# Performance work log

Hardware: AMD Instinct MI355X
Metric: run time of the kernel (lower is better)

The kernel has to match this reference:

```python
import jax, jax.numpy as jnp
import numpy as np

REALSHAPE = (32, 256, 256)   # even dims required
SHAPE = (32, 256, 129)       # rfft half-spectrum shape
MIDS = (16, 128, 128)
KCUT = 4
B, C = 4, 3


def _hs_np(f):
    # numpy mirror of Fourier.hermitian_symmetric (used only to build the constant feed mask)
    m0, m1, m2 = MIDS
    f = f.copy()
    f[m0+1:, 0, 0] = f[1:m0, 0, 0][::-1].conj()
    f[m0+1:, 0, m2] = f[1:m0, 0, m2][::-1].conj()
    f[m0+1:, m1, 0] = f[1:m0, m1, 0][::-1].conj()
    f[m0+1:, m1, m2] = f[1:m0, m1, m2][::-1].conj()
    f[0, m1+1:, 0] = f[0, 1:m1, 0][::-1].conj()
    f[0, m1+1:, m2] = f[0, 1:m1, m2][::-1].conj()
    f[m0, m1+1:, 0] = f[m0, 1:m1, 0][::-1].conj()
    f[m0, m1+1:, m2] = f[m0, 1:m1, m2][::-1].conj()
    f[m0+1:, m1+1:, 0] = f[1:m0, 1:m1, 0][::-1, ::-1].conj()
    f[m0+1:, 1:m1, 0] = f[1:m0, m1+1:, 0][::-1, ::-1].conj()
    f[m0+1:, m1+1:, m2] = f[1:m0, 1:m1, m2][::-1, ::-1].conj()
    f[m0+1:, 1:m1, m2] = f[1:m0, m1+1:, m2][::-1, ::-1].conj()
    return f


def _constants():
    ks = [np.fft.fftfreq(d, 1.0 / d) for d in SHAPE[:-1]] + [np.arange(SHAPE[-1])]
    kgrid = np.array(np.meshgrid(*ks, indexing='ij'))
    ksq = np.sum(kgrid ** 2, axis=0)
    holders = np.stack(np.meshgrid(*[np.arange(d) for d in SHAPE], indexing='ij'))
    same = np.all(np.stack([_hs_np(h) for h in holders]) == holders, axis=0)
    rem = same & (ksq <= KCUT ** 2)
    feed = np.stack([rem, rem.copy()])
    m0, m1, m2 = MIDS
    for idx in [(0, 0, 0), (0, 0, m2), (0, m1, 0), (0, m1, m2),
                (m0, 0, 0), (m0, 0, m2), (m0, m1, 0), (m0, m1, m2)]:
        feed[(1,) + idx] = False  # purely real corner modes
    feed_idx = np.nonzero(feed.reshape(-1))[0].astype(np.int32)
    ks_sel = np.stack([ksq, ksq])[feed]  # dimscale = (1,1,1)
    Pk = (1.0 / (ks_sel + 1.0) * float(np.prod(REALSHAPE))).astype(np.float32)
    grid = np.stack(np.meshgrid(*[np.arange(d) for d in REALSHAPE], indexing='ij')).astype(np.float32)
    return feed_idx, Pk, grid


def setup_inputs() -> dict:
    feed_idx, Pk, grid = _constants()
    key = jax.random.key(0)
    k1, k2 = jax.random.split(key)
    fr = jax.random.normal(k1, (B, C) + REALSHAPE, jnp.float32)
    seeds = jax.random.normal(k2, (1, 3 * feed_idx.size), jnp.float32)
    return {
        'fr': fr,
        'seeds': seeds,
        'Pk': jnp.asarray(Pk),
        'defscale': jnp.ones(3, jnp.float32),  # defscale / dimscale
        'grid': jnp.asarray(grid),
        'feed_idx': jnp.asarray(feed_idx),
    }


def _hs(f):
    # jax hermitian-symmetrize the rfft half-spectrum (writes are non-overlapping with reads)
    m0, m1, m2 = MIDS
    fl = lambda a: jnp.flip(a, 0).conj()
    fl2 = lambda a: jnp.flip(a, (0, 1)).conj()
    f = f.at[m0+1:, 0, 0].set(fl(f[1:m0, 0, 0]))
    f = f.at[m0+1:, 0, m2].set(fl(f[1:m0, 0, m2]))
    f = f.at[m0+1:, m1, 0].set(fl(f[1:m0, m1, 0]))
    f = f.at[m0+1:, m1, m2].set(fl(f[1:m0, m1, m2]))
    f = f.at[0, m1+1:, 0].set(fl(f[0, 1:m1, 0]))
    f = f.at[0, m1+1:, m2].set(fl(f[0, 1:m1, m2]))
    f = f.at[m0, m1+1:, 0].set(fl(f[m0, 1:m1, 0]))
    f = f.at[m0, m1+1:, m2].set(fl(f[m0, 1:m1, m2]))
    f = f.at[m0+1:, m1+1:, 0].set(fl2(f[1:m0, 1:m1, 0]))
    f = f.at[m0+1:, 1:m1, 0].set(fl2(f[1:m0, m1+1:, 0]))
    f = f.at[m0+1:, m1+1:, m2].set(fl2(f[1:m0, 1:m1, m2]))
    f = f.at[m0+1:, 1:m1, m2].set(fl2(f[1:m0, m1+1:, m2]))
    return f


def _forward(fr, seeds, Pk, defscale, grid, feed_idx):
    fdim = feed_idx.shape[0]
    # scale sparse coefficients by the power spectrum
    x = seeds.reshape(3, fdim) * Pk[None, :] * defscale[:, None]
    # scatter into the (2, *SHAPE) re/im spectrum via flat indices
    nfull = 2 * int(np.prod(SHAPE))
    arr = jnp.zeros((3, nfull), jnp.float32).at[:, feed_idx].set(x).reshape(3, 2, *SHAPE)
    comp = (arr[:, 0] + 1j * arr[:, 1]).astype(jnp.complex64)
    comp = jax.vmap(_hs)(comp)
    disp = jnp.fft.irfftn(comp[None], s=REALSHAPE, axes=(2, 3, 4))  # (1,3,D,H,W) float32
    D, H, W = REALSHAPE
    norm = (jnp.asarray(REALSHAPE, jnp.float32) - 1.0)[None, :, None, None, None]
    moved = 2.0 * ((grid[None] - disp) / norm) - 1.0  # normalized coords in [-1,1]
    gz, gy, gx = moved[0, 0], moved[0, 1], moved[0, 2]  # torch grid channel order [2,1,0] -> (x=W, y=H, z=D)
    # grid_sample: bilinear, padding_mode='border' (clamp float coords), align_corners=True
    fz = jnp.clip((gz + 1.0) * 0.5 * (D - 1), 0.0, D - 1)
    fy = jnp.clip((gy + 1.0) * 0.5 * (H - 1), 0.0, H - 1)
    fx = jnp.clip((gx + 1.0) * 0.5 * (W - 1), 0.0, W - 1)
    z0 = jnp.floor(fz); y0 = jnp.floor(fy); x0 = jnp.floor(fx)
    wz = fz - z0; wy = fy - y0; wx = fx - x0  # (D,H,W), broadcast against (B,C,D,H,W)
    z0i = z0.astype(jnp.int32); z1i = jnp.minimum(z0i + 1, D - 1)
    y0i = y0.astype(jnp.int32); y1i = jnp.minimum(y0i + 1, H - 1)
    x0i = x0.astype(jnp.int32); x1i = jnp.minimum(x0i + 1, W - 1)
    g = lambda zi, yi, xi: fr[:, :, zi, yi, xi]  # gather -> (B,C,D,H,W)
    c00 = g(z0i, y0i, x0i) * (1 - wx) + g(z0i, y0i, x1i) * wx
    c01 = g(z0i, y1i, x0i) * (1 - wx) + g(z0i, y1i, x1i) * wx
    c10 = g(z1i, y0i, x0i) * (1 - wx) + g(z1i, y0i, x1i) * wx
    c11 = g(z1i, y1i, x0i) * (1 - wx) + g(z1i, y1i, x1i) * wx
    c0 = c00 * (1 - wy) + c01 * wy
    c1 = c10 * (1 - wy) + c11 * wy
    return c0 * (1 - wz) + c1 * wz


def reference(fr, seeds, Pk, defscale, grid, feed_idx):
    return _forward(fr, seeds, Pk, defscale, grid, feed_idx)
```

## Files before the change

### kernel.cpp

```cpp
#include <hip/hip_runtime.h>
#include <math.h>

#define D0 32
#define D1 256
#define D2 256
#define HS2 129
#define NVOX (D0*D1*D2)
#define KMAX 4
#define NK 9
#define NK2 5
#define NCH 3
#define BATCH 4
#define FCH 3
#define NBC (BATCH*FCH)
#define C_FLOATS (NCH*NK*NK*NK2*2)

__global__ __launch_bounds__(256) void build_S(
    const float* __restrict__ seeds, const float* __restrict__ Pk,
    const float* __restrict__ defscale, const int* __restrict__ feed_idx,
    int fdim, float* __restrict__ S)
{
    __shared__ float C[C_FLOATS];
    __shared__ int fed[NK*NK];
    int t = threadIdx.x;
    for (int i = t; i < C_FLOATS; i += 256) C[i] = 0.0f;
    if (t < NK*NK) fed[t] = 0;
    __syncthreads();
    float ds0 = defscale[0], ds1 = defscale[1], ds2 = defscale[2];
    const int STR_RI = D0 * D1 * HS2;
    const int STR_A  = D1 * HS2;
    for (int j = t; j < fdim; j += 256) {
        int idx = feed_idx[j];
        int ri = idx / STR_RI; int r = idx - ri * STR_RI;
        int a  = r / STR_A;    r -= a * STR_A;
        int b  = r / HS2;      int c = r - b * HS2;
        int k0 = (a < D0/2) ? a : a - D0;
        int k1 = (b < D1/2) ? b : b - D1;
        if (k0 < -KMAX || k0 > KMAX || k1 < -KMAX || k1 > KMAX || c > KMAX) continue;
        int i0 = k0 + KMAX, i1 = k1 + KMAX;
        float pk = Pk[j];
        int base = ((i0*NK + i1)*NK2 + c)*2 + ri;
        C[base]                 = seeds[0*fdim + j] * pk * ds0;
        C[base + 1*NK*NK*NK2*2] = seeds[1*fdim + j] * pk * ds1;
        C[base + 2*NK*NK*NK2*2] = seeds[2*fdim + j] * pk * ds2;
        if (c == 0) fed[i0*NK + i1] = 1;
    }
    __syncthreads();
    if (t < NK*NK && !fed[t]) {
        int i0 = t / NK, i1 = t - i0*NK;
        int m0 = (NK-1) - i0, m1 = (NK-1) - i1;
        for (int ch = 0; ch < NCH; ++ch) {
            int dst = ((ch*NK*NK + i0*NK + i1)*NK2 + 0)*2;
            int src = ((ch*NK*NK + m0*NK + m1)*NK2 + 0)*2;
            C[dst]   = C[src];
            C[dst+1] = -C[src+1];
        }
    }
    __syncthreads();

    int zyl = t >> 3;
    int g   = t & 7;
    int zy = blockIdx.x * 32 + zyl;
    int z = zy >> 8, y = zy & 255;

    float w0r[NK], w0i[NK], w1r[NK], w1i[NK];
    {
        float th = (float)z * (6.28318530717958647692f / (float)D0);
        float sb, cb; __sincosf(th, &sb, &cb);
        w0r[KMAX] = 1.0f; w0i[KMAX] = 0.0f;
        float pr = 1.0f, pi = 0.0f;
        #pragma unroll
        for (int k = 1; k <= KMAX; ++k) {
            float nr = pr*cb - pi*sb, ni = pr*sb + pi*cb;
            pr = nr; pi = ni;
            w0r[KMAX+k] = pr; w0i[KMAX+k] = pi;
            w0r[KMAX-k] = pr; w0i[KMAX-k] = -pi;
        }
    }
    {
        float th = (float)y * (6.28318530717958647692f / (float)D1);
        float sb, cb; __sincosf(th, &sb, &cb);
        w1r[KMAX] = 1.0f; w1i[KMAX] = 0.0f;
        float pr = 1.0f, pi = 0.0f;
        #pragma unroll
        for (int k = 1; k <= KMAX; ++k) {
            float nr = pr*cb - pi*sb, ni = pr*sb + pi*cb;
            pr = nr; pi = ni;
            w1r[KMAX+k] = pr; w1i[KMAX+k] = pi;
            w1r[KMAX-k] = pr; w1i[KMAX-k] = -pi;
        }
    }

    float Sr[NCH*NK2], Si[NCH*NK2];
    #pragma unroll
    for (int i = 0; i < NCH*NK2; ++i) { Sr[i] = 0.0f; Si[i] = 0.0f; }

    for (int m = g; m < NK*NK; m += 8) {
        int i0 = m / NK, i1 = m - i0*NK;
        float Tr = w0r[i0]*w1r[i1] - w0i[i0]*w1i[i1];
        float Ti = w0r[i0]*w1i[i1] + w0i[i0]*w1r[i1];
        const float* Cp = C + m*NK2*2;
        #pragma unroll
        for (int ch = 0; ch < NCH; ++ch) {
            #pragma unroll
            for (int k2 = 0; k2 < NK2; ++k2) {
                float cr = Cp[ch*(NK*NK*NK2*2) + k2*2];
                float ci = Cp[ch*(NK*NK*NK2*2) + k2*2 + 1];
                int o = ch*NK2 + k2;
                Sr[o] += cr*Tr - ci*Ti;
                Si[o] += cr*Ti + ci*Tr;
            }
        }
    }

    #pragma unroll
    for (int off = 4; off >= 1; off >>= 1) {
        #pragma unroll
        for (int i = 0; i < NCH*NK2; ++i) {
            Sr[i] += __shfl_down(Sr[i], off, 8);
            Si[i] += __shfl_down(Si[i], off, 8);
        }
    }

    if (g == 0) {
        const float invN = 1.0f / (float)NVOX;
        #pragma unroll
        for (int ch = 0; ch < NCH; ++ch) {
            #pragma unroll
            for (int k2 = 0; k2 < NK2; ++k2) {
                int o = ch*NK2 + k2;
                float sc = (k2 == 0) ? invN : 2.0f*invN;
                S[(o*2 + 0)*8192 + zy] = Sr[o] * sc;
                S[(o*2 + 1)*8192 + zy] = Si[o] * sc;
            }
        }
    }
}

__global__ __launch_bounds__(256) void deform_sample(
    const float* __restrict__ fr, const float* __restrict__ S,
    float* __restrict__ out)
{
    int i = blockIdx.x;
    int xcd = i & 7;
    int j = i >> 3;
    int zyl = j / NBC;
    int bc  = j - zyl * NBC;
    int zy  = (xcd << 10) + zyl;
    int z = zy >> 8, y = zy & 255;
    int x = threadIdx.x;

    float s0r[NCH], skr[NCH][KMAX], ski[NCH][KMAX];
    #pragma unroll
    for (int ch = 0; ch < NCH; ++ch) {
        s0r[ch] = S[((ch*NK2 + 0)*2 + 0)*8192 + zy];
        #pragma unroll
        for (int k = 1; k <= KMAX; ++k) {
            skr[ch][k-1] = S[((ch*NK2 + k)*2 + 0)*8192 + zy];
            ski[ch][k-1] = S[((ch*NK2 + k)*2 + 1)*8192 + zy];
        }
    }

    float th = (float)x * (6.28318530717958647692f / (float)D2);
    float sb, cb; __sincosf(th, &sb, &cb);
    float ckr[KMAX], cks[KMAX];
    ckr[0] = cb; cks[0] = sb;
    #pragma unroll
    for (int k = 1; k < KMAX; ++k) {
        float nr = ckr[k-1]*cb - cks[k-1]*sb;
        float ni = cks[k-1]*cb + ckr[k-1]*sb;
        ckr[k] = nr; cks[k] = ni;
    }

    float d[NCH];
    #pragma unroll
    for (int ch = 0; ch < NCH; ++ch) {
        float acc = s0r[ch];
        #pragma unroll
        for (int k = 0; k < KMAX; ++k)
            acc += skr[ch][k]*ckr[k] - ski[ch][k]*cks[k];
        d[ch] = acc;
    }

    float fz = fminf(fmaxf((float)z - d[0], 0.0f), (float)(D0-1));
    float fy = fminf(fmaxf((float)y - d[1], 0.0f), (float)(D1-1));
    float fx = fminf(fmaxf((float)x - d[2], 0.0f), (float)(D2-1));

    float z0f = floorf(fz), y0f = floorf(fy), x0f = floorf(fx);
    int z0 = (int)z0f, y0 = (int)y0f, x0 = (int)x0f;
    int z1 = min(z0 + 1, D0-1), y1 = min(y0 + 1, D1-1), x1 = min(x0 + 1, D2-1);
    float wz = fz - z0f, wy = fy - y0f, wx = fx - x0f;
    float wz0 = 1.0f - wz, wy0 = 1.0f - wy, wx0 = 1.0f - wx;

    const float* __restrict__ v = fr + ((size_t)bc << 21);
    int o00 = (z0 << 16) + (y0 << 8);
    int o01 = (z0 << 16) + (y1 << 8);
    int o10 = (z1 << 16) + (y0 << 8);
    int o11 = (z1 << 16) + (y1 << 8);

    float v000 = v[o00 + x0], v001 = v[o00 + x1];
    float v010 = v[o01 + x0], v011 = v[o01 + x1];
    float v100 = v[o10 + x0], v101 = v[o10 + x1];
    float v110 = v[o11 + x0], v111 = v[o11 + x1];

    float c00 = v000*wx0 + v001*wx;
    float c01 = v010*wx0 + v011*wx;
    float c10 = v100*wx0 + v101*wx;
    float c11 = v110*wx0 + v111*wx;
    float c0 = c00*wy0 + c01*wy;
    float c1 = c10*wy0 + c11*wy;

    __builtin_nontemporal_store(c0*wz0 + c1*wz,
        &out[((size_t)bc << 21) + (zy << 8) + x]);
}

extern "C" void kernel_launch(void* const* d_in, const int* in_sizes, int n_in,
                              void* d_out, int out_size, void* d_ws, size_t ws_size,
                              hipStream_t stream) {
    const float* fr       = (const float*)d_in[0];
    const float* seeds    = (const float*)d_in[1];
    const float* Pk       = (const float*)d_in[2];
    const float* defscale = (const float*)d_in[3];
    const int*   feed_idx = (const int*)d_in[5];
    int fdim = in_sizes[2];

    float* S = (float*)d_ws;

    build_S<<<256, 256, 0, stream>>>(seeds, Pk, defscale, feed_idx, fdim, S);
    deform_sample<<<8192*NBC, 256, 0, stream>>>(fr, S, (float*)d_out);
}
```

Measured before the change: 324.8 us.

## Process all three channels per thread and remap blocks by batch and z-half

Each block now handles one (z,y) row for one batch across all three feature channels, so the displacement field and interpolation weights are computed once and reused for three gathers instead of being recomputed per channel. The grid shrinks to a third, and the block-to-XCD mapping changes so each XCD handles one batch and one half of z rather than a contiguous zy range across all channels. This cuts redundant S loads and trig/weight arithmetic but changes which data each XCD's L2 caches, which may affect gather locality.

```diff
diff --git a/kernel.cpp b/kernel.cpp
--- a/kernel.cpp
+++ b/kernel.cpp
@@ -142,12 +142,13 @@
     float* __restrict__ out)
 {
     int i = blockIdx.x;
-    int xcd = i & 7;
+    int u = i & 7;
+    int b  = u >> 1;
+    int zh = u & 1;
     int j = i >> 3;
-    int zyl = j / NBC;
-    int bc  = j - zyl * NBC;
-    int zy  = (xcd << 10) + zyl;
-    int z = zy >> 8, y = zy & 255;
+    int z = (zh << 4) + (j >> 8);
+    int y = j & 255;
+    int zy = (z << 8) + y;
     int x = threadIdx.x;
 
     float s0r[NCH], skr[NCH][KMAX], ski[NCH][KMAX];
@@ -192,26 +193,27 @@
     float wz = fz - z0f, wy = fy - y0f, wx = fx - x0f;
     float wz0 = 1.0f - wz, wy0 = 1.0f - wy, wx0 = 1.0f - wx;
 
-    const float* __restrict__ v = fr + ((size_t)bc << 21);
     int o00 = (z0 << 16) + (y0 << 8);
     int o01 = (z0 << 16) + (y1 << 8);
     int o10 = (z1 << 16) + (y0 << 8);
     int o11 = (z1 << 16) + (y1 << 8);
 
-    float v000 = v[o00 + x0], v001 = v[o00 + x1];
-    float v010 = v[o01 + x0], v011 = v[o01 + x1];
-    float v100 = v[o10 + x0], v101 = v[o10 + x1];
-    float v110 = v[o11 + x0], v111 = v[o11 + x1];
-
-    float c00 = v000*wx0 + v001*wx;
-    float c01 = v010*wx0 + v011*wx;
-    float c10 = v100*wx0 + v101*wx;
-    float c11 = v110*wx0 + v111*wx;
-    float c0 = c00*wy0 + c01*wy;
-    float c1 = c10*wy0 + c11*wy;
-
-    __builtin_nontemporal_store(c0*wz0 + c1*wz,
-        &out[((size_t)bc << 21) + (zy << 8) + x]);
+    const float* __restrict__ v0p = fr + ((size_t)(b*3 + 0) << 21);
+    const float* __restrict__ v1p = fr + ((size_t)(b*3 + 1) << 21);
+    const float* __restrict__ v2p = fr + ((size_t)(b*3 + 2) << 21);
+    size_t ob = ((size_t)(b*3) << 21) + (zy << 8) + x;
+
+    #pragma unroll
+    for (int c = 0; c < 3; ++c) {
+        const float* __restrict__ v = (c == 0) ? v0p : (c == 1) ? v1p : v2p;
+        float c00 = v[o00 + x0]*wx0 + v[o00 + x1]*wx;
+        float c01 = v[o01 + x0]*wx0 + v[o01 + x1]*wx;
+        float c10 = v[o10 + x0]*wx0 + v[o10 + x1]*wx;
+        float c11 = v[o11 + x0]*wx0 + v[o11 + x1]*wx;
+        float cc0 = c00*wy0 + c01*wy;
+        float cc1 = c10*wy0 + c11*wy;
+        __builtin_nontemporal_store(cc0*wz0 + cc1*wz, &out[ob + ((size_t)c << 21)]);
+    }
 }
 
 extern "C" void kernel_launch(void* const* d_in, const int* in_sizes, int n_in,
@@ -227,5 +229,5 @@
     float* S = (float*)d_ws;
 
     build_S<<<256, 256, 0, stream>>>(seeds, Pk, defscale, feed_idx, fdim, S);
-    deform_sample<<<8192*NBC, 256, 0, stream>>>(fr, S, (float*)d_out);
+    deform_sample<<<8192*4, 256, 0, stream>>>(fr, S, (float*)d_out);
 }
```

Result: faster. 311.5 us (-4.1%).
